# Optimization experiments

Hardware: AMD Instinct MI355X
Metric: run time of the kernel (lower is better)

## Reference

```python
import jax, jax.numpy as jnp
import numpy as np

B = 64
N_TEXT, N_VIS, N_AC = 256, 32, 32
N = N_TEXT + N_VIS + N_AC  # 320 total graph nodes
HID, HEADS, LAYERS = 512, 8, 2
HEAD_DIM = HID // HEADS
SW_K, SW_P, SF_M, ALPHA, CROSS_P = 6, 0.15, 3, 0.5, 0.3


def build_hybrid_adj():
    """Watts-Strogatz + Barabasi-Albert hybrid adjacency with cross-modal edges (numpy, setup only)."""
    rng = np.random.default_rng(0)
    # small-world ring lattice
    sw = np.zeros((N, N), np.float32)
    idx = np.arange(N)
    for j in range(1, SW_K // 2 + 1):
        sw[idx, (idx + j) % N] = 1.0
        sw[idx, (idx - j) % N] = 1.0
    # rewiring
    for i in range(N):
        for j in range(i + 1, N):
            if sw[i, j] == 1 and rng.random() < SW_P:
                sw[i, j] = sw[j, i] = 0.0
                cand = np.where(sw[i] == 0)[0]
                cand = cand[cand != i]
                if len(cand) > 0:
                    nj = rng.choice(cand)
                    sw[i, nj] = sw[nj, i] = 1.0
    # scale-free (Barabasi-Albert)
    sf = np.zeros((N, N), np.float32)
    for i in range(SF_M + 1):
        for j in range(i + 1, SF_M + 1):
            sf[i, j] = sf[j, i] = 1.0
    deg = sf.sum(1)
    for v in range(SF_M + 1, N):
        prob = deg[:v] / deg[:v].sum()
        targets = rng.choice(v, size=min(SF_M, v), replace=False, p=prob)
        sf[v, targets] = 1.0
        sf[targets, v] = 1.0
        deg = sf.sum(1)
    adj = ((ALPHA * sw + (1.0 - ALPHA) * sf) > 0.3).astype(np.float32)
    # cross-modal edges: text<->visual, text<->acoustic (Bernoulli), visual<->acoustic temporal diagonal
    ts, te = 0, N_TEXT
    vs, ve = te, te + N_VIS
    as_, ae = ve, ve + N_AC
    cm_v = (rng.random((N_TEXT, N_VIS)) < CROSS_P).astype(np.float32)
    adj[ts:te, vs:ve] = np.maximum(adj[ts:te, vs:ve], cm_v)
    adj[vs:ve, ts:te] = adj[ts:te, vs:ve].T
    cm_a = (rng.random((N_TEXT, N_AC)) < CROSS_P).astype(np.float32)
    adj[ts:te, as_:ae] = np.maximum(adj[ts:te, as_:ae], cm_a)
    adj[as_:ae, ts:te] = adj[ts:te, as_:ae].T
    k = min(N_VIS, N_AC)
    adj[vs + np.arange(k), as_ + np.arange(k)] = 1.0
    adj[as_ + np.arange(k), vs + np.arange(k)] = 1.0
    return adj.astype(np.int32)


def setup_inputs() -> dict:
    key = jax.random.key(0)
    ks = jax.random.split(key, 12)
    s = 0.02
    return {
        "text": jax.random.normal(ks[0], (B, N_TEXT, 768), jnp.float32),
        "visual": jax.random.normal(ks[1], (B, N_VIS, 47), jnp.float32),
        "acoustic": jax.random.normal(ks[2], (B, N_AC, 74), jnp.float32),
        "adj": jnp.asarray(build_hybrid_adj()),
        "Wt": jax.random.normal(ks[3], (768, HID), jnp.float32) * s,
        "Wv": jax.random.normal(ks[4], (47, HID), jnp.float32) * s,
        "Wa": jax.random.normal(ks[5], (74, HID), jnp.float32) * s,
        "Wg": jax.random.normal(ks[6], (LAYERS, HEADS, HID, HEAD_DIM), jnp.float32) * s,
        "a_src": jax.random.normal(ks[7], (LAYERS, HEADS, HEAD_DIM), jnp.float32) * s,
        "a_dst": jax.random.normal(ks[8], (LAYERS, HEADS, HEAD_DIM), jnp.float32) * s,
        "edge_logits": jax.random.normal(ks[9], (N, N), jnp.float32) * s,
    }


def _fusion(text, visual, acoustic, adj, Wt, Wv, Wa, Wg, a_src, a_dst, edge_logits):
    # project each modality into shared hidden space and stack as graph nodes
    x = jnp.concatenate([
        jnp.einsum("btd,dh->bth", text, Wt),
        jnp.einsum("bvd,dh->bvh", visual, Wv),
        jnp.einsum("bad,dh->bah", acoustic, Wa),
    ], axis=1)  # [B, N, HID]
    mask = (adj != 0)[None, None, :, :]  # [1,1,N,N]
    for l in range(LAYERS):
        h = jnp.einsum("bnd,hdf->bhnf", x, Wg[l])          # [B,H,N,Fh]
        # a([h_i || h_j]) factorizes: e_ij = a_src.h_i + a_dst.h_j
        fi = jnp.einsum("bhnf,hf->bhn", h, a_src[l])
        fj = jnp.einsum("bhnf,hf->bhn", h, a_dst[l])
        e = jax.nn.leaky_relu(fi[:, :, :, None] + fj[:, :, None, :], 0.2)
        e = e + edge_logits[None, None, :, :]               # learnable topology bias
        e = jnp.where(mask, e, -jnp.inf)                    # adjacency-masked scores
        att = jnp.nan_to_num(jax.nn.softmax(e, axis=-1))    # fully-masked rows -> 0
        out = jnp.einsum("bhij,bhjf->bhif", att, h)         # message passing
        x = out.transpose(0, 2, 1, 3).reshape(x.shape[0], N, HID)  # concat heads
        if l < LAYERS - 1:
            x = jax.nn.elu(x)
    return x  # [B, N, HID] fused node embeddings


def reference(text, visual, acoustic, adj, Wt, Wv, Wa, Wg, a_src, a_dst, edge_logits):
    return _fusion(text, visual, acoustic, adj, Wt, Wv, Wa, Wg, a_src, a_dst, edge_logits)
```

## Files before the change

kernel.cpp:

```cpp
#include <hip/hip_runtime.h>
#include <hip/hip_bf16.h>
#include <math.h>

#define BB 64
#define NN 320
#define NT 256
#define NV 32
#define NA 32
#define HIDD 512
#define NHEAD 8
#define FD 64

typedef __attribute__((ext_vector_type(8))) short bf16x8;
typedef __attribute__((ext_vector_type(4))) float floatx4;

__device__ float me_g[NN * NN];
__device__ float fif_g[512 * NN];
__device__ float fjf_g[512 * NN];
__device__ unsigned short tihi_g[16384 * 768];
__device__ unsigned short tilo_g[16384 * 768];
__device__ unsigned short vihi_g[2048 * 64];
__device__ unsigned short vilo_g[2048 * 64];
__device__ unsigned short achi_g[2048 * 128];
__device__ unsigned short aclo_g[2048 * 128];
__device__ unsigned short xhi_g[20480 * 512];
__device__ unsigned short xlo_g[20480 * 512];
__device__ unsigned short bwhi_g[512 * 768];
__device__ unsigned short bwlo_g[512 * 768];

__device__ __forceinline__ void split1(float v, unsigned short& h, unsigned short& l) {
    unsigned u = __float_as_uint(v);
    unsigned hu = u & 0xFFFF0000u;
    float lf = v - __uint_as_float(hu);
    h = (unsigned short)(hu >> 16);
    l = (unsigned short)(__float_as_uint(lf) >> 16);
}
__device__ __forceinline__ unsigned pack2(unsigned short a, unsigned short b) {
    return (unsigned)a | ((unsigned)b << 16);
}

__global__ __launch_bounds__(256) void build_me(
    const int* __restrict__ adj, const float* __restrict__ elog)
{
    const int i4 = (blockIdx.x * 256 + threadIdx.x) * 4;
    const int4   a = *(const int4*)&adj[i4];
    const float4 e = *(const float4*)&elog[i4];
    float4 m;
    m.x = a.x ? __expf(e.x) : 0.f;
    m.y = a.y ? __expf(e.y) : 0.f;
    m.z = a.z ? __expf(e.z) : 0.f;
    m.w = a.w ? __expf(e.w) : 0.f;
    *(float4*)&me_g[i4] = m;
}

__global__ __launch_bounds__(256) void presplit_A(
    const float* __restrict__ src, int M, int K, int nk, int sel)
{
    unsigned short* dh = (sel == 0) ? tihi_g : (sel == 1) ? vihi_g : achi_g;
    unsigned short* dl = (sel == 0) ? tilo_g : (sel == 1) ? vilo_g : aclo_g;
    const unsigned t = blockIdx.x * 256 + threadIdx.x;
    const unsigned lane = t & 63, rec = t >> 6;
    const unsigned kt = rec % (unsigned)nk, g = rec / (unsigned)nk;
    const int row = g * 16 + (lane & 15);
    if (row >= M) return;
    const int k0 = kt * 32 + ((lane >> 4) << 3);
    float v[8];
    if (((K & 3) == 0) && (k0 + 8 <= K)) {
        *(float4*)&v[0] = *(const float4*)&src[(size_t)row * K + k0];
        *(float4*)&v[4] = *(const float4*)&src[(size_t)row * K + k0 + 4];
    } else {
#pragma unroll
        for (int e = 0; e < 8; e++) v[e] = (k0 + e < K) ? src[(size_t)row * K + k0 + e] : 0.f;
    }
    unsigned short h[8], l[8];
#pragma unroll
    for (int e = 0; e < 8; e++) split1(v[e], h[e], l[e]);
    const size_t o = (size_t)t * 8;
    *(uint4*)&dh[o] = make_uint4(pack2(h[0],h[1]), pack2(h[2],h[3]),
                                 pack2(h[4],h[5]), pack2(h[6],h[7]));
    *(uint4*)&dl[o] = make_uint4(pack2(l[0],l[1]), pack2(l[2],l[3]),
                                 pack2(l[4],l[5]), pack2(l[6],l[7]));
}

__global__ __launch_bounds__(64) void presplit_B(
    const float* __restrict__ W, int K, int Kp, int wg_mode)
{
    const int lane = threadIdx.x;
    const int nt = blockIdx.x, kt = blockIdx.y;
    const int col = nt * 16 + (lane & 15);
    const int k0 = kt * 32 + (lane >> 4) * 8;
    unsigned short h[8], l[8];
#pragma unroll
    for (int e = 0; e < 8; e++) {
        const int k = k0 + e;
        float v = 0.f;
        if (k < K) v = wg_mode ? W[(size_t)(col >> 6) * (512 * 64) + (size_t)k * 64 + (col & 63)]
                               : W[(size_t)k * 512 + col];
        split1(v, h[e], l[e]);
    }
    const size_t o = (((size_t)nt * (Kp >> 5) + kt) * 64 + lane) * 8;
    *(uint4*)&bwhi_g[o] = make_uint4(pack2(h[0], h[1]), pack2(h[2], h[3]),
                                     pack2(h[4], h[5]), pack2(h[6], h[7]));
    *(uint4*)&bwlo_g[o] = make_uint4(pack2(l[0], l[1]), pack2(l[2], l[3]),
                                     pack2(l[4], l[5]), pack2(l[6], l[7]));
}

#define GLOAD(AH, AL, BH, BL, KT)                                              \
  { _Pragma("unroll") for (int s = 0; s < 4; s++) {                            \
      const unsigned ao = ((gbase + s) * (unsigned)nk + (KT)) * 512 + la8;     \
      AH[s] = *(const bf16x8*)&Ahi[ao];                                        \
      AL[s] = *(const bf16x8*)&Alo[ao]; }                                      \
    _Pragma("unroll") for (int t = 0; t < 4; t++) {                            \
      const unsigned bo = ((tgb + t) * (unsigned)nk + (KT)) * 512 + la8;       \
      BH[t] = *(const bf16x8*)&bwhi_g[bo];                                     \
      BL[t] = *(const bf16x8*)&bwlo_g[bo]; } }

#define GMFMA(AH, AL, BH, BL)                                                  \
  _Pragma("unroll") for (int s = 0; s < 4; s++)                                \
  _Pragma("unroll") for (int t = 0; t < 4; t++) {                              \
      acc[s][t] = __builtin_amdgcn_mfma_f32_16x16x32_bf16(AH[s], BH[t], acc[s][t], 0, 0, 0); \
      acc[s][t] = __builtin_amdgcn_mfma_f32_16x16x32_bf16(AH[s], BL[t], acc[s][t], 0, 0, 0); \
      acc[s][t] = __builtin_amdgcn_mfma_f32_16x16x32_bf16(AL[s], BH[t], acc[s][t], 0, 0, 0); }

__global__ __launch_bounds__(256, 2) void gemm_reg(
    unsigned short* __restrict__ Hthi, unsigned short* __restrict__ Htlo,
    const float* __restrict__ asrc, const float* __restrict__ adst,
    int nk, int a_sel, int b_mode, int rpb, int noff)
{
    __shared__ float slab[4][16][68];

    const unsigned short* Ahi = (a_sel == 0) ? tihi_g : (a_sel == 1) ? vihi_g
                              : (a_sel == 2) ? achi_g : xhi_g;
    const unsigned short* Alo = (a_sel == 0) ? tilo_g : (a_sel == 1) ? vilo_g
                              : (a_sel == 2) ? aclo_g : xlo_g;

    const int tid = threadIdx.x, lane = tid & 63, w = tid >> 6;
    const int rw = w >> 1, cw = w & 1;
    const int m0 = blockIdx.x * 128, n0 = blockIdx.y * 128;
    const unsigned gbase = (unsigned)(m0 >> 4) + rw * 4;
    const unsigned tgb   = (unsigned)(n0 >> 4) + cw * 4;
    const unsigned la8   = (unsigned)lane * 8;

    floatx4 acc[4][4];
#pragma unroll
    for (int s = 0; s < 4; s++)
#pragma unroll
        for (int t = 0; t < 4; t++) acc[s][t] = (floatx4)0.f;

    bf16x8 ahE[4], alE[4], bhE[4], blE[4];
    bf16x8 ahO[4], alO[4], bhO[4], blO[4];

    GLOAD(ahE, alE, bhE, blE, 0u);
    for (int kt = 0; kt < nk; kt += 2) {
        GLOAD(ahO, alO, bhO, blO, (unsigned)(kt + 1));
        GMFMA(ahE, alE, bhE, blE);
        if (kt + 2 < nk) GLOAD(ahE, alE, bhE, blE, (unsigned)(kt + 2));
        GMFMA(ahO, alO, bhO, blO);
    }

    const int fq = lane & 15, rl = lane >> 4;

    if (b_mode == 0) {
        float (*sl)[68] = slab[w];
        const int ktg0 = (n0 + cw * 64) >> 5;
#pragma unroll
        for (int s = 0; s < 4; s++) {
#pragma unroll
            for (int t = 0; t < 4; t++)
#pragma unroll
                for (int r = 0; r < 4; r++)
                    sl[rl * 4 + r][t * 16 + fq] = acc[s][t][r];
            const int grow16 = m0 + rw * 64 + s * 16;
            const int b = grow16 / rpb;
            const int rr = grow16 - b * rpb;
            const unsigned g = (unsigned)b * 20 + (unsigned)((noff + rr) >> 4);
#pragma unroll
            for (int kth = 0; kth < 2; kth++) {
                float f[8];
                *(float4*)&f[0] = *(const float4*)&sl[fq][kth * 32 + rl * 8];
                *(float4*)&f[4] = *(const float4*)&sl[fq][kth * 32 + rl * 8 + 4];
                unsigned short h[8], l[8];
#pragma unroll
                for (int e = 0; e < 8; e++) split1(f[e], h[e], l[e]);
                const size_t o = (((size_t)g * 16 + ktg0 + kth) * 64 + lane) * 8;
                *(uint4*)&xhi_g[o] = make_uint4(pack2(h[0],h[1]), pack2(h[2],h[3]),
                                                pack2(h[4],h[5]), pack2(h[6],h[7]));
                *(uint4*)&xlo_g[o] = make_uint4(pack2(l[0],l[1]), pack2(l[2],l[3]),
                                                pack2(l[4],l[5]), pack2(l[6],l[7]));
            }
        }
    } else {
        const int hd = (n0 + cw * 64) >> 6;
#pragma unroll
        for (int s = 0; s < 4; s++) {
            const int m_s = m0 + rw * 64 + s * 16 + rl * 4;
            const unsigned b = (unsigned)m_s / 320u;
            const int jb = m_s - b * 320;
            const int ks = jb >> 5;
            const int jg2 = (jb >> 3) & 3;
            const int eb = jb & 7;
            const size_t slabo = (size_t)b * 8 + hd;
#pragma unroll
            for (int t = 0; t < 4; t++) {
                unsigned short h0,h1,h2,h3,l0,l1,l2,l3;
                split1(acc[s][t][0],h0,l0); split1(acc[s][t][1],h1,l1);
                split1(acc[s][t][2],h2,l2); split1(acc[s][t][3],h3,l3);
                const size_t base = (((slabo * 10 + ks) * 4 + t) * 512
                                     + (size_t)(fq | (jg2 << 4)) * 8) + eb;
                *(uint2*)&Hthi[base] = make_uint2(pack2(h0,h1), pack2(h2,h3));
                *(uint2*)&Htlo[base] = make_uint2(pack2(l0,l1), pack2(l2,l3));
            }
        }
        float as4[4], ad4[4];
#pragma unroll
        for (int t = 0; t < 4; t++) {
            as4[t] = asrc[hd * 64 + t * 16 + fq];
            ad4[t] = adst[hd * 64 + t * 16 + fq];
        }
#pragma unroll
        for (int s = 0; s < 4; s++) {
            const int m_s = m0 + rw * 64 + s * 16 + rl * 4;
            const unsigned b = (unsigned)m_s / 320u;
            const int jb = m_s - b * 320;
            float4 fi4, fj4;
#pragma unroll
            for (int r = 0; r < 4; r++) {
                float fi = (acc[s][0][r]*as4[0] + acc[s][1][r]*as4[1])
                         + (acc[s][2][r]*as4[2] + acc[s][3][r]*as4[3]);
                float fj = (acc[s][0][r]*ad4[0] + acc[s][1][r]*ad4[1])
                         + (acc[s][2][r]*ad4[2] + acc[s][3][r]*ad4[3]);
#pragma unroll
                for (int d = 1; d < 16; d <<= 1) {
                    fi += __shfl_xor(fi, d);
                    fj += __shfl_xor(fj, d);
                }
                ((float*)&fi4)[r] = fi; ((float*)&fj4)[r] = fj;
            }
            if (fq == 0) {
                const size_t o = ((size_t)b * 8 + hd) * NN + jb;
                *(float4*)&fif_g[o] = fi4;
                *(float4*)&fjf_g[o] = fj4;
            }
        }
    }
}

template<int IP0, int NIP>
__device__ __forceinline__ void attn_body(
    const unsigned short* __restrict__ Hthi, const unsigned short* __restrict__ Htlo,
    float* __restrict__ xout, int final_out, float* fjs, float* ls,
    float (*slabA)[16][68])
{
    const int bh = blockIdx.x;
    const int hd = bh & 7, b = bh >> 3;
    const int tid = threadIdx.x, lane = tid & 63, w = tid >> 6;
    const int fq = lane & 15, jg = lane >> 4;

    for (int r = tid; r < NN; r += 256) fjs[r] = fjf_g[bh * NN + r];

    float fir[NIP];
#pragma unroll
    for (int ip = 0; ip < NIP; ip++)
        fir[ip] = fif_g[bh * NN + (IP0 + ip) * 64 + (w << 4) + fq];
    __syncthreads();

    floatx4 acc[NIP][4];
#pragma unroll
    for (int ip = 0; ip < NIP; ip++)
#pragma unroll
        for (int nt = 0; nt < 4; nt++) acc[ip][nt] = (floatx4)0.f;
    float lacc[NIP];
#pragma unroll
    for (int ip = 0; ip < NIP; ip++) lacc[ip] = 0.f;

    for (int ks = 0; ks < 10; ks++) {
        const int j8 = ks * 32 + jg * 8;
        const float4 fj0 = *(const float4*)&fjs[j8];
        const float4 fj1 = *(const float4*)&fjs[j8 + 4];

        bf16x8 ahh[NIP], all[NIP];
#pragma unroll
        for (int ip = 0; ip < NIP; ip++) {
            const int i = (IP0 + ip) * 64 + (w << 4) + fq;
            const float fiv = fir[ip];
            const unsigned g = (unsigned)i * NN + j8;
            const float4 m0 = *(const float4*)&me_g[g];
            const float4 m1 = *(const float4*)&me_g[g + 4];
            float p[8];
            {
                float s;
                s = fiv + fj0.x; s = fmaxf(s, 0.2f*s); p[0] = __expf(s) * m0.x;
                s = fiv + fj0.y; s = fmaxf(s, 0.2f*s); p[1] = __expf(s) * m0.y;
                s = fiv + fj0.z; s = fmaxf(s, 0.2f*s); p[2] = __expf(s) * m0.z;
                s = fiv + fj0.w; s = fmaxf(s, 0.2f*s); p[3] = __expf(s) * m0.w;
                s = fiv + fj1.x; s = fmaxf(s, 0.2f*s); p[4] = __expf(s) * m1.x;
                s = fiv + fj1.y; s = fmaxf(s, 0.2f*s); p[5] = __expf(s) * m1.y;
                s = fiv + fj1.z; s = fmaxf(s, 0.2f*s); p[6] = __expf(s) * m1.z;
                s = fiv + fj1.w; s = fmaxf(s, 0.2f*s); p[7] = __expf(s) * m1.w;
            }
            lacc[ip] += ((p[0]+p[1]) + (p[2]+p[3])) + ((p[4]+p[5]) + (p[6]+p[7]));

            unsigned short ph[8], pl[8];
#pragma unroll
            for (int e = 0; e < 8; e++) split1(p[e], ph[e], pl[e]);
            union { uint4 u; bf16x8 v; } ua, ul;
            ua.u = make_uint4(pack2(ph[0],ph[1]), pack2(ph[2],ph[3]),
                              pack2(ph[4],ph[5]), pack2(ph[6],ph[7]));
            ul.u = make_uint4(pack2(pl[0],pl[1]), pack2(pl[2],pl[3]),
                              pack2(pl[4],pl[5]), pack2(pl[6],pl[7]));
            ahh[ip] = ua.v; all[ip] = ul.v;
        }

#pragma unroll
        for (int nt = 0; nt < 4; nt++) {
            const unsigned off = (((unsigned)bh * 10 + ks) * 4 + nt) * 512 + (unsigned)lane * 8;
            const bf16x8 bhf = *(const bf16x8*)&Hthi[off];
            const bf16x8 blf = *(const bf16x8*)&Htlo[off];
#pragma unroll
            for (int ip = 0; ip < NIP; ip++) {
                acc[ip][nt] = __builtin_amdgcn_mfma_f32_16x16x32_bf16(ahh[ip], bhf, acc[ip][nt], 0, 0, 0);
                acc[ip][nt] = __builtin_amdgcn_mfma_f32_16x16x32_bf16(ahh[ip], blf, acc[ip][nt], 0, 0, 0);
                acc[ip][nt] = __builtin_amdgcn_mfma_f32_16x16x32_bf16(all[ip], bhf, acc[ip][nt], 0, 0, 0);
            }
        }
    }

#pragma unroll
    for (int ip = 0; ip < NIP; ip++) {
        float l = lacc[ip];
        l += __shfl_xor(l, 16);
        l += __shfl_xor(l, 32);
        if (jg == 0) ls[(IP0 + ip) * 64 + (w << 4) + fq] = l;
    }
    __syncthreads();

    if (final_out) {
#pragma unroll
        for (int ip = 0; ip < NIP; ip++) {
            const int ib = ((IP0 + ip) * 4 + w) * 16 + jg * 4;
#pragma unroll
            for (int r = 0; r < 4; r++) {
                const float lv = ls[ib + r];
                const float inv = (lv > 0.f) ? 1.f / lv : 0.f;
                const size_t ro = ((size_t)(b * NN + ib + r)) * HIDD + hd * 64;
#pragma unroll
                for (int nt = 0; nt < 4; nt++)
                    xout[ro + nt * 16 + fq] = acc[ip][nt][r] * inv;
            }
        }
    } else {
        float (*sl)[68] = slabA[w];
        const int ktg0 = hd * 2;
#pragma unroll
        for (int ip = 0; ip < NIP; ip++) {
            const int ib = ((IP0 + ip) * 4 + w) * 16 + jg * 4;
#pragma unroll
            for (int r = 0; r < 4; r++) {
                const float lv = ls[ib + r];
                const float inv = (lv > 0.f) ? 1.f / lv : 0.f;
#pragma unroll
                for (int nt = 0; nt < 4; nt++) {
                    float vv = acc[ip][nt][r] * inv;
                    vv = (vv > 0.f) ? vv : __expf(vv) - 1.f;
                    sl[jg * 4 + r][nt * 16 + fq] = vv;
                }
            }
            const unsigned g = (unsigned)b * 20 + (IP0 + ip) * 4 + w;
#pragma unroll
            for (int kth = 0; kth < 2; kth++) {
                float f[8];
                *(float4*)&f[0] = *(const float4*)&sl[fq][kth * 32 + jg * 8];
                *(float4*)&f[4] = *(const float4*)&sl[fq][kth * 32 + jg * 8 + 4];
                unsigned short h[8], l[8];
#pragma unroll
                for (int e = 0; e < 8; e++) split1(f[e], h[e], l[e]);
                const size_t o = (((size_t)g * 16 + ktg0 + kth) * 64 + lane) * 8;
                *(uint4*)&xhi_g[o] = make_uint4(pack2(h[0],h[1]), pack2(h[2],h[3]),
                                                pack2(h[4],h[5]), pack2(h[6],h[7]));
                *(uint4*)&xlo_g[o] = make_uint4(pack2(l[0],l[1]), pack2(l[2],l[3]),
                                                pack2(l[4],l[5]), pack2(l[6],l[7]));
            }
        }
    }
}

__global__ __launch_bounds__(256, 4) void attn_mfma(
    const unsigned short* __restrict__ Hthi, const unsigned short* __restrict__ Htlo,
    float* __restrict__ xout, int final_out)
{
    __shared__ float fjs[NN];
    __shared__ float ls[NN];
    __shared__ float slabA[4][16][68];
    if (blockIdx.y == 0) attn_body<0, 3>(Hthi, Htlo, xout, final_out, fjs, ls, slabA);
    else                 attn_body<3, 2>(Hthi, Htlo, xout, final_out, fjs, ls, slabA);
}

extern "C" void kernel_launch(void* const* d_in, const int* in_sizes, int n_in,
                              void* d_out, int out_size, void* d_ws, size_t ws_size,
                              hipStream_t stream)
{
    (void)in_sizes; (void)n_in; (void)out_size; (void)ws_size;
    const float* text     = (const float*)d_in[0];
    const float* visual   = (const float*)d_in[1];
    const float* acoustic = (const float*)d_in[2];
    const int*   adj      = (const int*)d_in[3];
    const float* Wt       = (const float*)d_in[4];
    const float* Wv       = (const float*)d_in[5];
    const float* Wa       = (const float*)d_in[6];
    const float* Wg       = (const float*)d_in[7];
    const float* a_src    = (const float*)d_in[8];
    const float* a_dst    = (const float*)d_in[9];
    const float* elog     = (const float*)d_in[10];

    float* xbuf = (float*)d_out;
    unsigned short* Hthi = (unsigned short*)d_ws;
    unsigned short* Htlo = Hthi + (size_t)512 * 10 * 4 * 512;

    build_me<<<NN * NN / 1024, 256, 0, stream>>>(adj, elog);

    presplit_A<<<(16384 / 16) * 24 * 64 / 256, 256, 0, stream>>>(text,     16384, 768, 24, 0);
    presplit_A<<<(2048  / 16) * 2  * 64 / 256, 256, 0, stream>>>(visual,   2048,  47,  2,  1);
    presplit_A<<<(2048  / 16) * 4  * 64 / 256, 256, 0, stream>>>(acoustic, 2048,  74,  4,  2);

    presplit_B<<<dim3(32, 768 / 32), 64, 0, stream>>>(Wt, 768, 768, 0);
    gemm_reg<<<dim3((BB*NT)/128, 4), 256, 0, stream>>>(nullptr, nullptr, nullptr, nullptr,
                                                       24, 0, 0, NT, 0);
    presplit_B<<<dim3(32, 64 / 32), 64, 0, stream>>>(Wv, 47, 64, 0);
    gemm_reg<<<dim3((BB*NV)/128, 4), 256, 0, stream>>>(nullptr, nullptr, nullptr, nullptr,
                                                       2, 1, 0, NV, NT);
    presplit_B<<<dim3(32, 128 / 32), 64, 0, stream>>>(Wa, 74, 128, 0);
    gemm_reg<<<dim3((BB*NA)/128, 4), 256, 0, stream>>>(nullptr, nullptr, nullptr, nullptr,
                                                       4, 2, 0, NA, NT + NV);

    for (int l = 0; l < 2; l++) {
        const float* Wg_l = Wg + (size_t)l * NHEAD * HIDD * FD;
        presplit_B<<<dim3(32, 512 / 32), 64, 0, stream>>>(Wg_l, 512, 512, 1);
        gemm_reg<<<dim3((BB*NN)/128, 4), 256, 0, stream>>>(Hthi, Htlo,
            a_src + l * NHEAD * FD, a_dst + l * NHEAD * FD, 16, 3, 1, NN, 0);
        attn_mfma<<<dim3(BB * NHEAD, 2), 256, 0, stream>>>(
            Hthi, Htlo, xbuf, (l == 0) ? 0 : 1);
    }
}
```

Baseline: 367.8 us.

## Stage GEMM operand tiles through LDS via direct global-to-LDS loads

Replaces the register double-buffered GEMM, in which each wave loaded its own A and B fragments from global memory, with a kernel where each wave copies one operand plane (A hi/lo, B hi/lo) into a shared LDS stage using global_load_lds. All waves then read their fragments from LDS, so each tile is fetched from global memory once per block instead of once per wave that uses it. The epilogue reuses the stage buffer as scratch, and occupancy is raised to 3 blocks per SM. The new loop is single-buffered with two barriers per k-step, so load latency is no longer overlapped with MFMA work.

```diff
diff --git a/kernel.cpp b/kernel.cpp
--- a/kernel.cpp
+++ b/kernel.cpp
@@ -39,6 +39,14 @@
     return (unsigned)a | ((unsigned)b << 16);
 }
 
+typedef const __attribute__((address_space(1))) unsigned int* gas1_t;
+typedef __attribute__((address_space(3))) unsigned int* las3_t;
+__device__ __forceinline__ void gload_lds16(const void* g, void* s) {
+    __builtin_amdgcn_global_load_lds((gas1_t)(unsigned long long)g,
+                                     (las3_t)(unsigned)(unsigned long long)s,
+                                     16, 0, 0);
+}
+
 __global__ __launch_bounds__(256) void build_me(
     const int* __restrict__ adj, const float* __restrict__ elog)
 {
@@ -105,16 +113,6 @@
                                      pack2(l[4], l[5]), pack2(l[6], l[7]));
 }
 
-#define GLOAD(AH, AL, BH, BL, KT)                                              \
-  { _Pragma("unroll") for (int s = 0; s < 4; s++) {                            \
-      const unsigned ao = ((gbase + s) * (unsigned)nk + (KT)) * 512 + la8;     \
-      AH[s] = *(const bf16x8*)&Ahi[ao];                                        \
-      AL[s] = *(const bf16x8*)&Alo[ao]; }                                      \
-    _Pragma("unroll") for (int t = 0; t < 4; t++) {                            \
-      const unsigned bo = ((tgb + t) * (unsigned)nk + (KT)) * 512 + la8;       \
-      BH[t] = *(const bf16x8*)&bwhi_g[bo];                                     \
-      BL[t] = *(const bf16x8*)&bwlo_g[bo]; } }
-
 #define GMFMA(AH, AL, BH, BL)                                                  \
   _Pragma("unroll") for (int s = 0; s < 4; s++)                                \
   _Pragma("unroll") for (int t = 0; t < 4; t++) {                              \
@@ -122,12 +120,12 @@
       acc[s][t] = __builtin_amdgcn_mfma_f32_16x16x32_bf16(AH[s], BL[t], acc[s][t], 0, 0, 0); \
       acc[s][t] = __builtin_amdgcn_mfma_f32_16x16x32_bf16(AL[s], BH[t], acc[s][t], 0, 0, 0); }
 
-__global__ __launch_bounds__(256, 2) void gemm_reg(
+__global__ __launch_bounds__(256, 3) void gemm_lds(
     unsigned short* __restrict__ Hthi, unsigned short* __restrict__ Htlo,
     const float* __restrict__ asrc, const float* __restrict__ adst,
     int nk, int a_sel, int b_mode, int rpb, int noff)
 {
-    __shared__ float slab[4][16][68];
+    __shared__ __align__(16) unsigned short stage[32 * 512];
 
     const unsigned short* Ahi = (a_sel == 0) ? tihi_g : (a_sel == 1) ? vihi_g
                               : (a_sel == 2) ? achi_g : xhi_g;
@@ -137,9 +135,13 @@
     const int tid = threadIdx.x, lane = tid & 63, w = tid >> 6;
     const int rw = w >> 1, cw = w & 1;
     const int m0 = blockIdx.x * 128, n0 = blockIdx.y * 128;
-    const unsigned gbase = (unsigned)(m0 >> 4) + rw * 4;
-    const unsigned tgb   = (unsigned)(n0 >> 4) + cw * 4;
-    const unsigned la8   = (unsigned)lane * 8;
+    const int g0 = m0 >> 4, tg0 = n0 >> 4;
+
+    const unsigned short* plane = (w == 0) ? Ahi : (w == 1) ? Alo
+                                : (w == 2) ? bwhi_g : bwlo_g;
+    const unsigned rec0 = (w < 2) ? (unsigned)g0 : (unsigned)tg0;
+    const unsigned short* wsrc = plane + (size_t)rec0 * nk * 512 + lane * 8;
+    unsigned short* wdst = &stage[(w * 8) * 512];
 
     floatx4 acc[4][4];
 #pragma unroll
@@ -147,21 +149,32 @@
 #pragma unroll
         for (int t = 0; t < 4; t++) acc[s][t] = (floatx4)0.f;
 
-    bf16x8 ahE[4], alE[4], bhE[4], blE[4];
-    bf16x8 ahO[4], alO[4], bhO[4], blO[4];
-
-    GLOAD(ahE, alE, bhE, blE, 0u);
-    for (int kt = 0; kt < nk; kt += 2) {
-        GLOAD(ahO, alO, bhO, blO, (unsigned)(kt + 1));
-        GMFMA(ahE, alE, bhE, blE);
-        if (kt + 2 < nk) GLOAD(ahE, alE, bhE, blE, (unsigned)(kt + 2));
-        GMFMA(ahO, alO, bhO, blO);
+    for (int kt = 0; kt < nk; ++kt) {
+        __syncthreads();
+#pragma unroll
+        for (int u = 0; u < 8; u++)
+            gload_lds16(wsrc + ((size_t)u * nk + kt) * 512, wdst + u * 512);
+        __syncthreads();
+
+        bf16x8 a_h[4], a_l[4], b_h[4], b_l[4];
+#pragma unroll
+        for (int s = 0; s < 4; s++) {
+            a_h[s] = *(const bf16x8*)&stage[(rw * 4 + s) * 512 + lane * 8];
+            a_l[s] = *(const bf16x8*)&stage[(8 + rw * 4 + s) * 512 + lane * 8];
+        }
+#pragma unroll
+        for (int t = 0; t < 4; t++) {
+            b_h[t] = *(const bf16x8*)&stage[(16 + cw * 4 + t) * 512 + lane * 8];
+            b_l[t] = *(const bf16x8*)&stage[(24 + cw * 4 + t) * 512 + lane * 8];
+        }
+        GMFMA(a_h, a_l, b_h, b_l);
     }
 
     const int fq = lane & 15, rl = lane >> 4;
 
     if (b_mode == 0) {
-        float (*sl)[68] = slab[w];
+        __syncthreads();
+        float (*sl)[68] = (float (*)[68])(&stage[w * 2176]);
         const int ktg0 = (n0 + cw * 64) >> 5;
 #pragma unroll
         for (int s = 0; s < 4; s++) {
@@ -423,19 +436,19 @@
     presplit_A<<<(2048  / 16) * 4  * 64 / 256, 256, 0, stream>>>(acoustic, 2048,  74,  4,  2);
 
     presplit_B<<<dim3(32, 768 / 32), 64, 0, stream>>>(Wt, 768, 768, 0);
-    gemm_reg<<<dim3((BB*NT)/128, 4), 256, 0, stream>>>(nullptr, nullptr, nullptr, nullptr,
+    gemm_lds<<<dim3((BB*NT)/128, 4), 256, 0, stream>>>(nullptr, nullptr, nullptr, nullptr,
                                                        24, 0, 0, NT, 0);
     presplit_B<<<dim3(32, 64 / 32), 64, 0, stream>>>(Wv, 47, 64, 0);
-    gemm_reg<<<dim3((BB*NV)/128, 4), 256, 0, stream>>>(nullptr, nullptr, nullptr, nullptr,
+    gemm_lds<<<dim3((BB*NV)/128, 4), 256, 0, stream>>>(nullptr, nullptr, nullptr, nullptr,
                                                        2, 1, 0, NV, NT);
     presplit_B<<<dim3(32, 128 / 32), 64, 0, stream>>>(Wa, 74, 128, 0);
-    gemm_reg<<<dim3((BB*NA)/128, 4), 256, 0, stream>>>(nullptr, nullptr, nullptr, nullptr,
+    gemm_lds<<<dim3((BB*NA)/128, 4), 256, 0, stream>>>(nullptr, nullptr, nullptr, nullptr,
                                                        4, 2, 0, NA, NT + NV);
 
     for (int l = 0; l < 2; l++) {
         const float* Wg_l = Wg + (size_t)l * NHEAD * HIDD * FD;
         presplit_B<<<dim3(32, 512 / 32), 64, 0, stream>>>(Wg_l, 512, 512, 1);
-        gemm_reg<<<dim3((BB*NN)/128, 4), 256, 0, stream>>>(Hthi, Htlo,
+        gemm_lds<<<dim3((BB*NN)/128, 4), 256, 0, stream>>>(Hthi, Htlo,
             a_src + l * NHEAD * FD, a_dst + l * NHEAD * FD, 16, 3, 1, NN, 0);
         attn_mfma<<<dim3(BB * NHEAD, 2), 256, 0, stream>>>(
             Hthi, Htlo, xbuf, (l == 0) ? 0 : 1);
```

Result: no change. 364.5 us (-0.9%).
